# Kernel tuning notes

Hardware: AMD Instinct MI355X
Metric: run time of the kernel (lower is better)

Reference implementation:

```python
import jax, jax.numpy as jnp
import numpy as np

T, N, E, D, OUT, L = 12, 10000, 160000, 128, 64, 2


def setup_inputs() -> dict:
    key = jax.random.key(0)
    ks = jax.random.split(key, 8)
    s = 1.0 / np.sqrt(D)
    x = jax.random.normal(ks[0], (T, N, D), jnp.float32)
    hidden_states = jax.random.normal(ks[1], (L, N, D), jnp.float32)
    src = jax.random.randint(ks[2], (E,), 0, N, dtype=jnp.int32)
    dst = jax.random.randint(ks[3], (E,), 0, N, dtype=jnp.int32)
    W_self = jax.random.normal(ks[4], (L, 6, D, D), jnp.float32) * s
    W_neigh = jax.random.normal(ks[5], (L, 6, D, D), jnp.float32) * s
    b = jnp.zeros((L, 6, D), jnp.float32)
    W_out = jax.random.normal(ks[6], (D, OUT), jnp.float32) * s
    b_out = jnp.zeros((OUT,), jnp.float32)
    return dict(x=x, hidden_states=hidden_states, W_self=W_self, W_neigh=W_neigh,
                b=b, W_out=W_out, b_out=b_out, src=src, dst=dst)


def reference(x, hidden_states, W_self, W_neigh, b, W_out, b_out, src, dst):
    n_nodes = x.shape[1]
    deg = jax.ops.segment_sum(jnp.ones_like(dst, jnp.float32), dst, num_segments=n_nodes)
    deg_inv = jnp.where(deg > 0, 1.0 / deg, 0.0)[:, None]  # [N,1]

    def agg(f):  # mean over in-neighbors (DGL update_all copy_u + mean)
        return jax.ops.segment_sum(f[src], dst, num_segments=n_nodes) * deg_inv

    # agg_seq=True: original concatenates all timesteps and does one update_all;
    # mean is per-feature, so this equals per-timestep neighbor means, vmapped.
    hN_all = jax.vmap(agg)(x)  # [T,N,D]

    def net(f, fN, i, Ws, Wn, bl):  # SAGE-mean style message-passing net
        return f @ Ws[i] + fN @ Wn[i] + bl[i]

    def cell(xin, h, hN_x, Ws, Wn, bl):
        if hN_x is None:
            hN_x = agg(xin)
        hN_h = agg(h)
        r = jax.nn.sigmoid(net(xin, hN_x, 0, Ws, Wn, bl) + net(h, hN_h, 1, Ws, Wn, bl))
        u = jax.nn.sigmoid(net(xin, hN_x, 2, Ws, Wn, bl) + net(h, hN_h, 3, Ws, Wn, bl))
        c = jnp.tanh(net(xin, hN_x, 4, Ws, Wn, bl) + net(h, hN_h, 5, Ws, Wn, bl))
        return u * h + (1.0 - u) * c  # note: r*h is dead code in the source

    def step(hidden, inp_t):
        x_t, hN_t = inp_t
        cur, hN = x_t, hN_t
        new_h = []
        for j in range(L):  # small fixed depth
            cur = cell(cur, hidden[j], hN, W_self[j], W_neigh[j], b[j])
            new_h.append(cur)
            hN = None  # h_N only used by first layer (as in source)
        out = cur @ W_out + b_out
        return jnp.stack(new_h), out

    hidden_final, outputs = jax.lax.scan(step, hidden_states, (x, hN_all))
    return outputs, hidden_final
```

## Files before the change

### kernel.cpp

```cpp
#include <hip/hip_runtime.h>

typedef unsigned short u16;
typedef unsigned int   u32;
typedef __attribute__((ext_vector_type(4))) float f32x4;
typedef __attribute__((ext_vector_type(8))) short s16x8;

#define TT 12
#define NN 10000
#define EE 160000
#define DD 128
#define OO 64

__device__ __forceinline__ u16 f2bf(float f) {
  union { float f; u32 u; } x; x.f = f;
  u32 r = x.u + 0x7FFFu + ((x.u >> 16) & 1u);
  return (u16)(r >> 16);
}
__device__ __forceinline__ float bf2f(u16 v) {
  union { u32 u; float f; } x; x.u = (u32)v << 16; return x.f;
}

__global__ __launch_bounds__(256) void prep_kernel(
    const float* __restrict__ x, const float* __restrict__ hs,
    const int* __restrict__ dst,
    const float* __restrict__ Wself, const float* __restrict__ Wneigh,
    const float* __restrict__ b, const float* __restrict__ Wout,
    u16* __restrict__ xb, float* __restrict__ h0f, u16* __restrict__ hb0,
    float* __restrict__ h1f, u16* __restrict__ hb1,
    int* __restrict__ deg, u16* __restrict__ Wp,
    float* __restrict__ biasbuf, u16* __restrict__ WoT,
    int nx8, int nh8half, int E) {
  int gid = blockIdx.x * 256 + threadIdx.x;
  const int NWP = 2 * 256 * 512;
  const int NPACK = NWP + 64 * 128 + 512;
  int cvtXEnd = NPACK + nx8;
  int cvtHEnd = cvtXEnd + 2 * nh8half;
  int cntEnd  = cvtHEnd + E;
  if (gid < NPACK) {
    int pg = gid;
    if (pg < NWP) {
      int j = pg >> 17;
      int rem = pg & 131071;
      int c = rem >> 9;
      int k = rem & 511;
      int seg = k >> 7, kd = k & 127;
      int cc = c & 127;
      int gate = (c < 128) ? (seg < 2 ? 2 : 3) : (seg < 2 ? 4 : 5);
      const float* M = (seg & 1) ? Wneigh : Wself;
      float v = M[((j * 6 + gate) * 128 + kd) * 128 + cc];
      Wp[pg] = f2bf(v);
    } else if (pg < NWP + 64 * 128) {
      int i = pg - NWP;
      int c = i >> 7, k = i & 127;
      WoT[i] = f2bf(Wout[k * OO + c]);
    } else {
      int i = pg - NWP - 64 * 128;
      int j = i >> 8, g = (i >> 7) & 1, d = i & 127;
      int g1 = g ? 4 : 2, g2 = g ? 5 : 3;
      biasbuf[i] = b[(j * 6 + g1) * 128 + d] + b[(j * 6 + g2) * 128 + d];
    }
  } else if (gid < cvtXEnd) {
    int i8 = gid - NPACK;
    float4 va = *(const float4*)(x + (size_t)i8 * 8);
    float4 vb = *(const float4*)(x + (size_t)i8 * 8 + 4);
    uint4 p;
    p.x = (u32)f2bf(va.x) | ((u32)f2bf(va.y) << 16);
    p.y = (u32)f2bf(va.z) | ((u32)f2bf(va.w) << 16);
    p.z = (u32)f2bf(vb.x) | ((u32)f2bf(vb.y) << 16);
    p.w = (u32)f2bf(vb.z) | ((u32)f2bf(vb.w) << 16);
    *(uint4*)(xb + (size_t)i8 * 8) = p;
  } else if (gid < cvtHEnd) {
    int j = gid - cvtXEnd;
    int half = (j >= nh8half);
    int jj = half ? j - nh8half : j;
    float4 va = ((const float4*)hs)[(size_t)j * 2];
    float4 vb = ((const float4*)hs)[(size_t)j * 2 + 1];
    float* fdst = half ? h1f : h0f;
    u16*   bdst = half ? hb1 : hb0;
    ((float4*)fdst)[(size_t)jj * 2]     = va;
    ((float4*)fdst)[(size_t)jj * 2 + 1] = vb;
    uint4 p;
    p.x = (u32)f2bf(va.x) | ((u32)f2bf(va.y) << 16);
    p.y = (u32)f2bf(va.z) | ((u32)f2bf(va.w) << 16);
    p.z = (u32)f2bf(vb.x) | ((u32)f2bf(vb.y) << 16);
    p.w = (u32)f2bf(vb.z) | ((u32)f2bf(vb.w) << 16);
    ((uint4*)bdst)[jj] = p;
  } else if (gid < cntEnd) {
    int e = gid - cvtHEnd;
    atomicAdd(&deg[dst[e]], 1);
  }
}

__global__ __launch_bounds__(1024) void scan_kernel(const int* __restrict__ deg,
                                                    int* __restrict__ offs,
                                                    float* __restrict__ dinv, int n) {
  __shared__ int lds_deg[10240];
  __shared__ int wsum[16];
  int tid = threadIdx.x;
  for (int i = tid; i < 10240; i += 1024) lds_deg[i] = (i < n) ? deg[i] : 0;
  __syncthreads();
  int base = tid * 10;
  int loc[10];
  int s = 0;
  #pragma unroll
  for (int k = 0; k < 10; ++k) { loc[k] = s; s += lds_deg[base + k]; }
  int lane = tid & 63;
  int incl = s;
  #pragma unroll
  for (int d = 1; d < 64; d <<= 1) {
    int t2 = __shfl_up(incl, d);
    if (lane >= d) incl += t2;
  }
  int wid = tid >> 6;
  if (lane == 63) wsum[wid] = incl;
  __syncthreads();
  int wpre = 0;
  for (int k = 0; k < wid; ++k) wpre += wsum[k];
  int excl = wpre + incl - s;
  #pragma unroll
  for (int k = 0; k < 10; ++k) {
    int idx = base + k;
    if (idx < n) {
      int d0 = lds_deg[idx];
      offs[idx] = excl + loc[k];
      dinv[idx] = (d0 > 0) ? 1.0f / (float)d0 : 0.0f;
    }
  }
  if (tid == 1023) offs[n] = excl + s;
}

__global__ __launch_bounds__(256) void fill_kernel(const int* __restrict__ src,
                                                   const int* __restrict__ dst,
                                                   const int* __restrict__ offs,
                                                   int* __restrict__ cursor,
                                                   int* __restrict__ csr, int E) {
  int e = blockIdx.x * 256 + threadIdx.x;
  if (e >= E) return;
  int d = dst[e];
  int pos = atomicAdd(&cursor[d], 1);
  csr[offs[d] + pos] = src[e] * 64;
}

__device__ __forceinline__ void agg_one(const int* __restrict__ offs,
                                        const int* __restrict__ csr,
                                        const float* __restrict__ dinv,
                                        const u32* __restrict__ S,
                                        u32* __restrict__ O,
                                        int node, int lane) {
  int nu = __builtin_amdgcn_readfirstlane(node);
  int e0 = offs[nu], e1 = offs[nu + 1];
  float di = dinv[nu];
  float xa = 0.f, ya = 0.f, xb_ = 0.f, yb_ = 0.f;
  float xc = 0.f, yc = 0.f, xd = 0.f, yd = 0.f;
  int e = e0;
  for (; e + 8 <= e1; e += 8) {
    int i0 = csr[e],     i1 = csr[e + 1], i2 = csr[e + 2], i3 = csr[e + 3];
    int i4 = csr[e + 4], i5 = csr[e + 5], i6 = csr[e + 6], i7 = csr[e + 7];
    u32 v0 = S[i0 + lane], v1 = S[i1 + lane], v2 = S[i2 + lane], v3 = S[i3 + lane];
    u32 v4 = S[i4 + lane], v5 = S[i5 + lane], v6 = S[i6 + lane], v7 = S[i7 + lane];
    xa  += bf2f((u16)v0) + bf2f((u16)v1);
    ya  += bf2f((u16)(v0 >> 16)) + bf2f((u16)(v1 >> 16));
    xb_ += bf2f((u16)v2) + bf2f((u16)v3);
    yb_ += bf2f((u16)(v2 >> 16)) + bf2f((u16)(v3 >> 16));
    xc  += bf2f((u16)v4) + bf2f((u16)v5);
    yc  += bf2f((u16)(v4 >> 16)) + bf2f((u16)(v5 >> 16));
    xd  += bf2f((u16)v6) + bf2f((u16)v7);
    yd  += bf2f((u16)(v6 >> 16)) + bf2f((u16)(v7 >> 16));
  }
  for (; e + 4 <= e1; e += 4) {
    int i0 = csr[e], i1 = csr[e + 1], i2 = csr[e + 2], i3 = csr[e + 3];
    u32 v0 = S[i0 + lane], v1 = S[i1 + lane], v2 = S[i2 + lane], v3 = S[i3 + lane];
    xa  += bf2f((u16)v0) + bf2f((u16)v1);
    ya  += bf2f((u16)(v0 >> 16)) + bf2f((u16)(v1 >> 16));
    xb_ += bf2f((u16)v2) + bf2f((u16)v3);
    yb_ += bf2f((u16)(v2 >> 16)) + bf2f((u16)(v3 >> 16));
  }
  for (; e < e1; ++e) {
    u32 v = S[csr[e] + lane];
    xa += bf2f((u16)v); ya += bf2f((u16)(v >> 16));
  }
  float sx = ((xa + xb_) + (xc + xd)) * di;
  float sy = ((ya + yb_) + (yc + yd)) * di;
  O[nu * 64 + lane] = (u32)f2bf(sx) | ((u32)f2bf(sy) << 16);
}

__global__ __launch_bounds__(256) void aggs_kernel(const int* __restrict__ offs,
                                                   const int* __restrict__ csr,
                                                   const float* __restrict__ dinv,
                                                   const u16* __restrict__ s,
                                                   u16* __restrict__ o, int N) {
  int node = blockIdx.x * 4 + (threadIdx.x >> 6);
  if (node >= N) return;
  agg_one(offs, csr, dinv, (const u32*)s, (u32*)o, node, threadIdx.x & 63);
}

__global__ __launch_bounds__(256) void aggx_kernel(const int* __restrict__ offs,
                                                   const int* __restrict__ csr,
                                                   const float* __restrict__ dinv,
                                                   const u16* __restrict__ xb,
                                                   u16* __restrict__ axb, int N) {
  int id = blockIdx.x;
  int t, grp;
  if (id < 20000) {
    t = id & 7;
    grp = id >> 3;
  } else {
    int j = id - 20000;
    int slot = j & 7;
    t = 8 + (slot & 3);
    grp = (slot >> 2) * 1250 + (j >> 3);
  }
  int node = grp * 4 + (threadIdx.x >> 6);
  if (node >= N) return;
  size_t yo = (size_t)t * N * 64;
  agg_one(offs, csr, dinv, (const u32*)xb + yo, (u32*)axb + yo, node, threadIdx.x & 63);
}

__global__ __launch_bounds__(256) void aggdual_kernel(const int* __restrict__ offs,
                                                      const int* __restrict__ csr,
                                                      const float* __restrict__ dinv,
                                                      const u16* __restrict__ s0,
                                                      const u16* __restrict__ s1,
                                                      u16* __restrict__ o0,
                                                      u16* __restrict__ o1, int N) {
  int b = blockIdx.x;
  int srcsel = (b >> 2) & 1;
  int idx = (b >> 3) * 4 + (b & 3);
  int node = idx * 4 + (threadIdx.x >> 6);
  if (node >= N) return;
  const u32* S = (const u32*)(srcsel ? s1 : s0);
  u32* O = (u32*)(srcsel ? o1 : o0);
  agg_one(offs, csr, dinv, S, O, node, threadIdx.x & 63);
}

template <int MODE>
__device__ __forceinline__ void cell_body(char* __restrict__ smem, int row0, int tid,
    const u16* __restrict__ s0, const u16* __restrict__ s1,
    const u16* __restrict__ s2, const u16* __restrict__ s3,
    const u16* __restrict__ W, const float* __restrict__ bias,
    const float* __restrict__ hin, float* __restrict__ hout, u16* __restrict__ hbout,
    const u16* __restrict__ WoT, const float* __restrict__ bout,
    float* __restrict__ outp, int N) {
  u16* As = (u16*)smem;
  u16* Bs = (u16*)(smem + 8192);
  const u16* srcs[4] = {s0, s1, s2, s3};
  int lane = tid & 63, w = tid >> 6;
  int wr = w & 3, wc = w >> 2;

  f32x4 accU[4], accC[4];
  #pragma unroll
  for (int n = 0; n < 4; ++n) { accU[n] = (f32x4){0,0,0,0}; accC[n] = (f32x4){0,0,0,0}; }

  #pragma unroll
  for (int kc = 0; kc < 8; ++kc) {
    {
      int r = tid >> 3, k8 = (tid & 7) * 8;
      const u16* sp = srcs[kc >> 1];
      int grow = row0 + r;
      uint4 v = make_uint4(0, 0, 0, 0);
      if (grow < N) v = *(const uint4*)(sp + (size_t)grow * DD + (kc & 1) * 64 + k8);
      int byte = (r * 128 + (tid & 7) * 16) ^ ((r & 7) << 4);
      *(uint4*)((char*)As + byte) = v;
    }
    #pragma unroll
    for (int it = 0; it < 4; ++it) {
      int id = it * 512 + tid;
      int c = id >> 3, k8 = (id & 7) * 8;
      uint4 v = *(const uint4*)(W + c * 512 + kc * 64 + k8);
      int byte = (c * 128 + (id & 7) * 16) ^ ((c & 7) << 4);
      *(uint4*)((char*)Bs + byte) = v;
    }
    __syncthreads();
    #pragma unroll
    for (int ks = 0; ks < 2; ++ks) {
      int arow = wr * 16 + (lane & 15);
      int abyte = (arow * 128 + ks * 64 + (lane >> 4) * 16) ^ ((arow & 7) << 4);
      s16x8 af = *(const s16x8*)((char*)As + abyte);
      #pragma unroll
      for (int n = 0; n < 4; ++n) {
        int cu = wc * 64 + n * 16 + (lane & 15);
        int bub = (cu * 128 + ks * 64 + (lane >> 4) * 16) ^ ((cu & 7) << 4);
        s16x8 bu = *(const s16x8*)((char*)Bs + bub);
        accU[n] = __builtin_amdgcn_mfma_f32_16x16x32_bf16(af, bu, accU[n], 0, 0, 0);
        int cc = cu + 128;
        int bcb = (cc * 128 + ks * 64 + (lane >> 4) * 16) ^ ((cc & 7) << 4);
        s16x8 bc = *(const s16x8*)((char*)Bs + bcb);
        accC[n] = __builtin_amdgcn_mfma_f32_16x16x32_bf16(af, bc, accC[n], 0, 0, 0);
      }
    }
    __syncthreads();
  }

  #pragma unroll
  for (int n = 0; n < 4; ++n) {
    int col = wc * 64 + n * 16 + (lane & 15);
    float bu = bias[col], bc = bias[128 + col];
    #pragma unroll
    for (int r = 0; r < 4; ++r) {
      int row = row0 + wr * 16 + (lane >> 4) * 4 + r;
      if (row < N) {
        float u = 1.0f / (1.0f + __expf(-(accU[n][r] + bu)));
        float cg = tanhf(accC[n][r] + bc);
        size_t idx = (size_t)row * DD + col;
        float hn = u * hin[idx] + (1.0f - u) * cg;
        hout[idx] = hn;
        u16 hnb = f2bf(hn);
        hbout[idx] = hnb;
        if constexpr (MODE == 2) {
          int rl = row - row0;
          int hbyte = (rl * 256 + col * 2) ^ ((rl & 7) << 4);
          *(u16*)(smem + hbyte) = hnb;
        }
      }
    }
  }
  if constexpr (MODE == 2) {
    #pragma unroll
    for (int it = 0; it < 2; ++it) {
      int id = it * 512 + tid;
      int c = id >> 4, kc8 = (id & 15) * 8;
      uint4 v = *(const uint4*)(WoT + c * 128 + kc8);
      int byte = (c * 256 + kc8 * 2) ^ ((c & 7) << 4);
      *(uint4*)(smem + 16384 + byte) = v;
    }
    __syncthreads();
    f32x4 ao[2] = {};
    #pragma unroll
    for (int ks = 0; ks < 4; ++ks) {
      int arow = wr * 16 + (lane & 15);
      int abyte = (arow * 256 + ks * 64 + (lane >> 4) * 16) ^ ((arow & 7) << 4);
      s16x8 af = *(const s16x8*)(smem + abyte);
      #pragma unroll
      for (int n = 0; n < 2; ++n) {
        int co = wc * 32 + n * 16 + (lane & 15);
        int bbyte = (co * 256 + ks * 64 + (lane >> 4) * 16) ^ ((co & 7) << 4);
        s16x8 bf = *(const s16x8*)(smem + 16384 + bbyte);
        ao[n] = __builtin_amdgcn_mfma_f32_16x16x32_bf16(af, bf, ao[n], 0, 0, 0);
      }
    }
    #pragma unroll
    for (int n = 0; n < 2; ++n) {
      int co = wc * 32 + n * 16 + (lane & 15);
      float bb = bout[co];
      #pragma unroll
      for (int r = 0; r < 4; ++r) {
        int row = row0 + wr * 16 + (lane >> 4) * 4 + r;
        if (row < N) outp[(size_t)row * OO + co] = ao[n][r] + bb;
      }
    }
  }
}

__global__ __launch_bounds__(512) void cell0_kernel(const u16* __restrict__ xbt,
                                                    const u16* __restrict__ axbt,
                                                    const u16* __restrict__ hb0c,
                                                    const u16* __restrict__ ah0,
                                                    const u16* __restrict__ W,
                                                    const float* __restrict__ bias,
                                                    const float* __restrict__ h0in,
                                                    float* __restrict__ h0out,
                                                    u16* __restrict__ hb0out, int N) {
  __shared__ __align__(16) char smem[40960];
  cell_body<3>(smem, blockIdx.x * 64, threadIdx.x, xbt, axbt, hb0c, ah0,
               W, bias, h0in, h0out, hb0out, nullptr, nullptr, nullptr, N);
}

template <int WITHC0>
__global__ __launch_bounds__(512) void step_kernel(const u16* __restrict__ xbn,
                                                   const u16* __restrict__ axbn,
                                                   const u16* __restrict__ hb0c,
                                                   const u16* __restrict__ ah0,
                                                   const u16* __restrict__ hb1r,
                                                   const u16* __restrict__ ah1,
                                                   const u16* __restrict__ Wp,
                                                   const float* __restrict__ biasbuf,
                                                   const float* __restrict__ h1in,
                                                   float* __restrict__ h1out,
                                                   u16* __restrict__ hb1w,
                                                   const float* __restrict__ h0in,
                                                   float* __restrict__ h0out,
                                                   u16* __restrict__ hb0out,
                                                   const u16* __restrict__ WoT,
                                                   const float* __restrict__ bout,
                                                   float* __restrict__ outp, int N) {
  __shared__ __align__(16) char smem[40960];
  int bx = blockIdx.x;
  int role = WITHC0 ? (bx & 1) : 0;
  int row0 = (WITHC0 ? (bx >> 1) : bx) * 64;
  if (role == 0) {
    cell_body<2>(smem, row0, threadIdx.x, hb0c, ah0, hb1r, ah1,
                 Wp + 131072, biasbuf + 256,
                 h1in, h1out, hb1w, WoT, bout, outp, N);
  } else {
    cell_body<3>(smem, row0, threadIdx.x, xbn, axbn, hb0c, ah0,
                 Wp, biasbuf,
                 h0in, h0out, hb0out, nullptr, nullptr, nullptr, N);
  }
}

extern "C" void kernel_launch(void* const* d_in, const int* in_sizes, int n_in,
                              void* d_out, int out_size, void* d_ws, size_t ws_size,
                              hipStream_t stream) {
  const float* x      = (const float*)d_in[0];
  const float* hs     = (const float*)d_in[1];
  const float* Wself  = (const float*)d_in[2];
  const float* Wneigh = (const float*)d_in[3];
  const float* b      = (const float*)d_in[4];
  const float* Wout   = (const float*)d_in[5];
  const float* bout   = (const float*)d_in[6];
  const int*   src    = (const int*)d_in[7];
  const int*   dst    = (const int*)d_in[8];
  float* out = (float*)d_out;

  const int N = NN, E = EE, D = DD, T = TT;

  char* ws = (char*)d_ws;
  size_t off = 0;
  auto alloc = [&](size_t bytes) -> void* {
    void* p = ws + off;
    off = (off + bytes + 255) & ~(size_t)255;
    return p;
  };
  int*   deg     = (int*)alloc(N * 4);
  int*   offs    = (int*)alloc((N + 1) * 4);
  int*   cursor  = (int*)alloc(N * 4);
  int*   csr     = (int*)alloc(E * 4);
  float* dinv    = (float*)alloc(N * 4);
  u16*   Wp      = (u16*)alloc(2 * 256 * 512 * 2);
  float* biasbuf = (float*)alloc(512 * 4);
  u16*   WoT     = (u16*)alloc(64 * 128 * 2);
  float* h0A     = (float*)alloc((size_t)N * D * 4);
  float* h0B     = (float*)alloc((size_t)N * D * 4);
  float* h1f     = (float*)alloc((size_t)N * D * 4);
  u16*   hb0A    = (u16*)alloc((size_t)N * D * 2);
  u16*   hb0B    = (u16*)alloc((size_t)N * D * 2);
  u16*   hb1     = (u16*)alloc((size_t)N * D * 2);
  u16*   ah0b    = (u16*)alloc((size_t)N * D * 2);
  u16*   ah1b    = (u16*)alloc((size_t)N * D * 2);
  u16*   xb      = (u16*)alloc((size_t)T * N * D * 2);
  u16*   axb     = (u16*)alloc((size_t)T * N * D * 2);

  float* h0f[2] = {h0A, h0B};
  u16*   hb0[2] = {hb0A, hb0B};
  float* hid0 = out + (size_t)T * N * OO;
  float* hid1 = hid0 + (size_t)N * D;

  hipMemsetAsync(deg, 0, N * 4, stream);
  hipMemsetAsync(cursor, 0, N * 4, stream);
  {
    int nx8 = T * N * D / 8, nh8half = N * D / 8;
    int NPACK = 2 * 256 * 512 + 64 * 128 + 512;
    int tot = NPACK + nx8 + 2 * nh8half + E;
    prep_kernel<<<(tot + 255) / 256, 256, 0, stream>>>(
        x, hs, dst, Wself, Wneigh, b, Wout,
        xb, h0A, hb0A, h1f, hb1, deg, Wp, biasbuf, WoT, nx8, nh8half, E);
  }
  scan_kernel<<<1, 1024, 0, stream>>>(deg, offs, dinv, N);
  fill_kernel<<<(E + 255) / 256, 256, 0, stream>>>(src, dst, offs, cursor, csr, E);

  int aggGrid = (N + 3) / 4;
  int mmGrid  = (N + 63) / 64;

  aggx_kernel<<<30000, 256, 0, stream>>>(offs, csr, dinv, xb, axb, N);
  aggs_kernel<<<aggGrid, 256, 0, stream>>>(offs, csr, dinv, hb0A, ah0b, N);
  cell0_kernel<<<mmGrid, 512, 0, stream>>>(xb, axb, hb0A, ah0b, Wp, biasbuf,
                                           h0A, h0B, hb0B, N);

  for (int t = 0; t < T; ++t) {
    u16* cur = hb0[(t + 1) & 1];
    aggdual_kernel<<<2 * aggGrid, 256, 0, stream>>>(offs, csr, dinv, cur, hb1,
                                                    ah0b, ah1b, N);
    if (t < T - 1) {
      float* h0o = (t == T - 2) ? hid0 : h0f[t & 1];
      step_kernel<1><<<2 * mmGrid, 512, 0, stream>>>(
          xb + (size_t)(t + 1) * N * D, axb + (size_t)(t + 1) * N * D,
          cur, ah0b, hb1, ah1b, Wp, biasbuf,
          h1f, h1f, hb1,
          h0f[(t + 1) & 1], h0o, hb0[t & 1],
          WoT, bout, out + (size_t)t * N * OO, N);
    } else {
      step_kernel<0><<<mmGrid, 512, 0, stream>>>(
          nullptr, nullptr,
          cur, ah0b, hb1, ah1b, Wp, biasbuf,
          h1f, hid1, hb1, nullptr, nullptr, nullptr,
          WoT, bout, out + (size_t)t * N * OO, N);
    }
  }
}
```

Measured before the change: 637.6 us.

## Use direct global-to-LDS loads, pre-swizzled weights, and half-wave edge-split aggregation

```diff
diff --git a/kernel.cpp b/kernel.cpp
--- a/kernel.cpp
+++ b/kernel.cpp
@@ -18,6 +18,12 @@
 }
 __device__ __forceinline__ float bf2f(u16 v) {
   union { u32 u; float f; } x; x.u = (u32)v << 16; return x.f;
+}
+
+__device__ __forceinline__ void gload_lds16(const u16* g, u16* l) {
+  __builtin_amdgcn_global_load_lds(
+      (const __attribute__((address_space(1))) u32*)(const void*)g,
+      (__attribute__((address_space(3))) u32*)(void*)l, 16, 0, 0);
 }
 
 __global__ __launch_bounds__(256) void prep_kernel(
@@ -39,16 +45,20 @@
   if (gid < NPACK) {
     int pg = gid;
     if (pg < NWP) {
-      int j = pg >> 17;
-      int rem = pg & 131071;
-      int c = rem >> 9;
-      int k = rem & 511;
-      int seg = k >> 7, kd = k & 127;
-      int cc = c & 127;
-      int gate = (c < 128) ? (seg < 2 ? 2 : 3) : (seg < 2 ? 4 : 5);
-      const float* M = (seg & 1) ? Wneigh : Wself;
-      float v = M[((j * 6 + gate) * 128 + kd) * 128 + cc];
-      Wp[pg] = f2bf(v);
+      int cc = pg & 127;
+      int kd = (pg >> 7) & 127;
+      int gm = (pg >> 14) & 7;
+      int j  = pg >> 17;
+      int gate = 2 + (gm & 3);
+      int neigh = gm >> 2;
+      const float* M = neigh ? Wneigh : Wself;
+      float v = M[(((j * 6) + gate) * 128 + kd) * 128 + cc];
+      int c = cc + ((gate >= 4) ? 128 : 0);
+      int seg = (gate & 1) * 2 + neigh;
+      int k = seg * 128 + kd;
+      int kc = k >> 6, k6 = k & 63;
+      int ksw = ((k6 & ~7) ^ ((c & 7) << 3)) | (k6 & 7);
+      Wp[(size_t)j * 131072 + c * 512 + kc * 64 + ksw] = f2bf(v);
     } else if (pg < NWP + 64 * 128) {
       int i = pg - NWP;
       int c = i >> 7, k = i & 127;
@@ -141,79 +151,92 @@
   csr[offs[d] + pos] = src[e] * 64;
 }
 
-__device__ __forceinline__ void agg_one(const int* __restrict__ offs,
-                                        const int* __restrict__ csr,
-                                        const float* __restrict__ dinv,
-                                        const u32* __restrict__ S,
-                                        u32* __restrict__ O,
-                                        int node, int lane) {
+__device__ __forceinline__ void acc4(u32 vx, u32 vy, float& a, float& b, float& c, float& d) {
+  a += bf2f((u16)vx); b += bf2f((u16)(vx >> 16));
+  c += bf2f((u16)vy); d += bf2f((u16)(vy >> 16));
+}
+
+__device__ __forceinline__ void agg_one2(const int* __restrict__ offs,
+                                         const int* __restrict__ csr,
+                                         const float* __restrict__ dinv,
+                                         const u32* __restrict__ S,
+                                         u32* __restrict__ O,
+                                         int node, int lane) {
   int nu = __builtin_amdgcn_readfirstlane(node);
   int e0 = offs[nu], e1 = offs[nu + 1];
   float di = dinv[nu];
-  float xa = 0.f, ya = 0.f, xb_ = 0.f, yb_ = 0.f;
-  float xc = 0.f, yc = 0.f, xd = 0.f, yd = 0.f;
+  int half = lane >> 5;
+  int col = (lane & 31) * 2;
+  float a0 = 0, b0 = 0, c0 = 0, d0 = 0, a1 = 0, b1 = 0, c1 = 0, d1 = 0;
   int e = e0;
   for (; e + 8 <= e1; e += 8) {
-    int i0 = csr[e],     i1 = csr[e + 1], i2 = csr[e + 2], i3 = csr[e + 3];
-    int i4 = csr[e + 4], i5 = csr[e + 5], i6 = csr[e + 6], i7 = csr[e + 7];
-    u32 v0 = S[i0 + lane], v1 = S[i1 + lane], v2 = S[i2 + lane], v3 = S[i3 + lane];
-    u32 v4 = S[i4 + lane], v5 = S[i5 + lane], v6 = S[i6 + lane], v7 = S[i7 + lane];
-    xa  += bf2f((u16)v0) + bf2f((u16)v1);
-    ya  += bf2f((u16)(v0 >> 16)) + bf2f((u16)(v1 >> 16));
-    xb_ += bf2f((u16)v2) + bf2f((u16)v3);
-    yb_ += bf2f((u16)(v2 >> 16)) + bf2f((u16)(v3 >> 16));
-    xc  += bf2f((u16)v4) + bf2f((u16)v5);
-    yc  += bf2f((u16)(v4 >> 16)) + bf2f((u16)(v5 >> 16));
-    xd  += bf2f((u16)v6) + bf2f((u16)v7);
-    yd  += bf2f((u16)(v6 >> 16)) + bf2f((u16)(v7 >> 16));
-  }
-  for (; e + 4 <= e1; e += 4) {
-    int i0 = csr[e], i1 = csr[e + 1], i2 = csr[e + 2], i3 = csr[e + 3];
-    u32 v0 = S[i0 + lane], v1 = S[i1 + lane], v2 = S[i2 + lane], v3 = S[i3 + lane];
-    xa  += bf2f((u16)v0) + bf2f((u16)v1);
-    ya  += bf2f((u16)(v0 >> 16)) + bf2f((u16)(v1 >> 16));
-    xb_ += bf2f((u16)v2) + bf2f((u16)v3);
-    yb_ += bf2f((u16)(v2 >> 16)) + bf2f((u16)(v3 >> 16));
-  }
-  for (; e < e1; ++e) {
-    u32 v = S[csr[e] + lane];
-    xa += bf2f((u16)v); ya += bf2f((u16)(v >> 16));
-  }
-  float sx = ((xa + xb_) + (xc + xd)) * di;
-  float sy = ((ya + yb_) + (yc + yd)) * di;
-  O[nu * 64 + lane] = (u32)f2bf(sx) | ((u32)f2bf(sy) << 16);
-}
-
-__global__ __launch_bounds__(256) void aggs_kernel(const int* __restrict__ offs,
-                                                   const int* __restrict__ csr,
-                                                   const float* __restrict__ dinv,
-                                                   const u16* __restrict__ s,
-                                                   u16* __restrict__ o, int N) {
-  int node = blockIdx.x * 4 + (threadIdx.x >> 6);
-  if (node >= N) return;
-  agg_one(offs, csr, dinv, (const u32*)s, (u32*)o, node, threadIdx.x & 63);
+    int p0 = csr[e],     p1 = csr[e + 1], p2 = csr[e + 2], p3 = csr[e + 3];
+    int p4 = csr[e + 4], p5 = csr[e + 5], p6 = csr[e + 6], p7 = csr[e + 7];
+    uint2 v0 = *(const uint2*)(S + (half ? p1 : p0) + col);
+    uint2 v1 = *(const uint2*)(S + (half ? p3 : p2) + col);
+    uint2 v2 = *(const uint2*)(S + (half ? p5 : p4) + col);
+    uint2 v3 = *(const uint2*)(S + (half ? p7 : p6) + col);
+    acc4(v0.x, v0.y, a0, b0, c0, d0);
+    acc4(v1.x, v1.y, a1, b1, c1, d1);
+    acc4(v2.x, v2.y, a0, b0, c0, d0);
+    acc4(v3.x, v3.y, a1, b1, c1, d1);
+  }
+  if (e + 4 <= e1) {
+    int p0 = csr[e], p1 = csr[e + 1], p2 = csr[e + 2], p3 = csr[e + 3];
+    uint2 v0 = *(const uint2*)(S + (half ? p1 : p0) + col);
+    uint2 v1 = *(const uint2*)(S + (half ? p3 : p2) + col);
+    acc4(v0.x, v0.y, a0, b0, c0, d0);
+    acc4(v1.x, v1.y, a1, b1, c1, d1);
+    e += 4;
+  }
+  if (e + 2 <= e1) {
+    int p0 = csr[e], p1 = csr[e + 1];
+    uint2 v0 = *(const uint2*)(S + (half ? p1 : p0) + col);
+    acc4(v0.x, v0.y, a0, b0, c0, d0);
+    e += 2;
+  }
+  if (e < e1) {
+    uint2 v0 = *(const uint2*)(S + csr[e] + col);
+    if (!half) acc4(v0.x, v0.y, a1, b1, c1, d1);
+  }
+  float sa = a0 + a1, sb = b0 + b1, sc = c0 + c1, sd = d0 + d1;
+  sa += __shfl_down(sa, 32);
+  sb += __shfl_down(sb, 32);
+  sc += __shfl_down(sc, 32);
+  sd += __shfl_down(sd, 32);
+  if (!half) {
+    uint2 o;
+    o.x = (u32)f2bf(sa * di) | ((u32)f2bf(sb * di) << 16);
+    o.y = (u32)f2bf(sc * di) | ((u32)f2bf(sd * di) << 16);
+    *(uint2*)(O + (size_t)nu * 64 + col) = o;
+  }
 }
 
 __global__ __launch_bounds__(256) void aggx_kernel(const int* __restrict__ offs,
                                                    const int* __restrict__ csr,
                                                    const float* __restrict__ dinv,
                                                    const u16* __restrict__ xb,
-                                                   u16* __restrict__ axb, int N) {
+                                                   u16* __restrict__ axb,
+                                                   const u16* __restrict__ hb0,
+                                                   u16* __restrict__ ah0, int N) {
   int id = blockIdx.x;
-  int t, grp;
+  const u32* S; u32* O; int grp;
   if (id < 20000) {
-    t = id & 7;
-    grp = id >> 3;
-  } else {
+    int t = id & 7; grp = id >> 3;
+    S = (const u32*)xb + (size_t)t * N * 64; O = (u32*)axb + (size_t)t * N * 64;
+  } else if (id < 30000) {
     int j = id - 20000;
     int slot = j & 7;
-    t = 8 + (slot & 3);
+    int t = 8 + (slot & 3);
     grp = (slot >> 2) * 1250 + (j >> 3);
+    S = (const u32*)xb + (size_t)t * N * 64; O = (u32*)axb + (size_t)t * N * 64;
+  } else {
+    grp = id - 30000;
+    S = (const u32*)hb0; O = (u32*)ah0;
   }
   int node = grp * 4 + (threadIdx.x >> 6);
   if (node >= N) return;
-  size_t yo = (size_t)t * N * 64;
-  agg_one(offs, csr, dinv, (const u32*)xb + yo, (u32*)axb + yo, node, threadIdx.x & 63);
+  agg_one2(offs, csr, dinv, S, O, node, threadIdx.x & 63);
 }
 
 __global__ __launch_bounds__(256) void aggdual_kernel(const int* __restrict__ offs,
@@ -230,7 +253,7 @@
   if (node >= N) return;
   const u32* S = (const u32*)(srcsel ? s1 : s0);
   u32* O = (u32*)(srcsel ? o1 : o0);
-  agg_one(offs, csr, dinv, S, O, node, threadIdx.x & 63);
+  agg_one2(offs, csr, dinv, S, O, node, threadIdx.x & 63);
 }
 
 template <int MODE>
@@ -255,20 +278,15 @@
   for (int kc = 0; kc < 8; ++kc) {
     {
       int r = tid >> 3, k8 = (tid & 7) * 8;
-      const u16* sp = srcs[kc >> 1];
-      int grow = row0 + r;
-      uint4 v = make_uint4(0, 0, 0, 0);
-      if (grow < N) v = *(const uint4*)(sp + (size_t)grow * DD + (kc & 1) * 64 + k8);
-      int byte = (r * 128 + (tid & 7) * 16) ^ ((r & 7) << 4);
-      *(uint4*)((char*)As + byte) = v;
+      int k8s = k8 ^ ((r & 7) << 3);
+      const u16* g = srcs[kc >> 1] + (size_t)(row0 + r) * DD + (kc & 1) * 64 + k8s;
+      gload_lds16(g, As + (tid & ~63) * 8);
     }
     #pragma unroll
     for (int it = 0; it < 4; ++it) {
       int id = it * 512 + tid;
-      int c = id >> 3, k8 = (id & 7) * 8;
-      uint4 v = *(const uint4*)(W + c * 512 + kc * 64 + k8);
-      int byte = (c * 128 + (id & 7) * 16) ^ ((c & 7) << 4);
-      *(uint4*)((char*)Bs + byte) = v;
+      const u16* g = W + (id >> 3) * 512 + kc * 64 + (id & 7) * 8;
+      gload_lds16(g, Bs + (it * 512 + (tid & ~63)) * 8);
     }
     __syncthreads();
     #pragma unroll
@@ -439,6 +457,7 @@
   u16*   ah1b    = (u16*)alloc((size_t)N * D * 2);
   u16*   xb      = (u16*)alloc((size_t)T * N * D * 2);
   u16*   axb     = (u16*)alloc((size_t)T * N * D * 2);
+  (void)alloc(65536);
 
   float* h0f[2] = {h0A, h0B};
   u16*   hb0[2] = {hb0A, hb0B};
@@ -461,8 +480,7 @@
   int aggGrid = (N + 3) / 4;
   int mmGrid  = (N + 63) / 64;
 
-  aggx_kernel<<<30000, 256, 0, stream>>>(offs, csr, dinv, xb, axb, N);
-  aggs_kernel<<<aggGrid, 256, 0, stream>>>(offs, csr, dinv, hb0A, ah0b, N);
+  aggx_kernel<<<32500, 256, 0, stream>>>(offs, csr, dinv, xb, axb, hb0A, ah0b, N);
   cell0_kernel<<<mmGrid, 512, 0, stream>>>(xb, axb, hb0A, ah0b, Wp, biasbuf,
                                            h0A, h0B, hb0B, N);
 
```

Result: faster. 620.6 us (-2.7%).
